# Kernel tuning notes

Measured on AMD Instinct MI355X. Metric: run time of the kernel, lower is better.

The kernel has to match this reference:

```python
import jax, jax.numpy as jnp
import numpy as np

BETA = 0.25


def setup_inputs() -> dict:
    key = jax.random.key(0)
    k1, k2 = jax.random.split(key)
    ze = jax.random.normal(k1, (16, 64, 64, 64), dtype=jnp.float32)  # (B, L, H, W)
    # codebook init mirrors uniform_(-1/K, 1/K)
    K = 1024
    emb = jax.random.uniform(k2, (K, 64), dtype=jnp.float32, minval=-1.0 / K, maxval=1.0 / K)
    return {"ze": ze, "emb": emb}


def reference(ze, emb):
    B, L, H, W = ze.shape
    K = emb.shape[0]
    # (B, H, W, L) -> (N, L)
    zf = jnp.transpose(ze, (0, 2, 3, 1)).reshape(-1, L)
    # squared euclidean distances (N, K)
    d = (jnp.sum(zf * zf, axis=1, keepdims=True)
         + jnp.sum(emb * emb, axis=1)
         - 2.0 * zf @ emb.T)
    idx = jnp.argmin(d, axis=1)  # (N,)
    # direct gather == one-hot @ emb
    z_q = jnp.transpose(emb[idx].reshape(B, H, W, L), (0, 3, 1, 2))
    loss = (jnp.mean((jax.lax.stop_gradient(z_q) - ze) ** 2)
            + BETA * jnp.mean((z_q - jax.lax.stop_gradient(ze)) ** 2))
    # straight-through estimator
    z_q_st = ze + jax.lax.stop_gradient(z_q - ze)
    # perplexity of code usage
    counts = jnp.zeros((K,), dtype=zf.dtype).at[idx].add(1.0)
    e_mean = counts / zf.shape[0]
    perplexity = jnp.exp(-jnp.sum(e_mean * jnp.log(e_mean + 1e-10)))
    return z_q_st, loss, idx.reshape(-1, 1)
```

## Files before the change

kernel.cpp:

```cpp
#include <hip/hip_runtime.h>

typedef short bf16x8 __attribute__((ext_vector_type(8)));
typedef float f32x4  __attribute__((ext_vector_type(4)));

#define CAP 12

#define WS_LOSS 0
#define WS_DONE 8
#define WS_EBF  64

#define L_EBF    0
#define L_MARG   131072
#define L_CCNT   132096
#define L_KCH    133120
#define L_ROWMAX 134144
#define L_CSLOT  136192
#define L_TOTAL  148480

__device__ __forceinline__ unsigned short f2bf(float f) {
    unsigned u = __float_as_uint(f);
    return (unsigned short)((u + 0x7fffu + ((u >> 16) & 1u)) >> 16);
}

__device__ __forceinline__ float np_pairwise_sumsq64(const float* a) {
    float r[8];
    #pragma unroll
    for (int j = 0; j < 8; ++j) r[j] = __fmul_rn(a[j], a[j]);
    #pragma unroll
    for (int i = 8; i < 64; i += 8)
        #pragma unroll
        for (int j = 0; j < 8; ++j)
            r[j] = __fadd_rn(r[j], __fmul_rn(a[i + j], a[i + j]));
    return __fadd_rn(
        __fadd_rn(__fadd_rn(r[0], r[1]), __fadd_rn(r[2], r[3])),
        __fadd_rn(__fadd_rn(r[4], r[5]), __fadd_rn(r[6], r[7])));
}

__global__ __launch_bounds__(256) void prep_kernel(
    const float* __restrict__ emb, unsigned short* __restrict__ ebf,
    float* __restrict__ loss, int* __restrict__ done)
{
    int k = blockIdx.x * 256 + threadIdx.x;
    if (k == 0) { *loss = 0.0f; *done = 0; }
    if (k < 1024) {
        float e[64];
        #pragma unroll
        for (int l = 0; l < 64; ++l) e[l] = emb[k * 64 + l];
        int tile = k >> 4, r = k & 15;
        #pragma unroll
        for (int j = 0; j < 8; ++j) {
            bf16x8 v;
            #pragma unroll
            for (int m = 0; m < 8; ++m) v[m] = (short)f2bf(e[j * 8 + m]);
            *(bf16x8*)(ebf + tile * 1024 + j * 128 + r * 8) = v;
        }
    }
}

__global__ __launch_bounds__(512)
__attribute__((amdgpu_waves_per_eu(2, 2)))
void vq_kernel(
    const float* __restrict__ ze, const float* __restrict__ emb,
    const unsigned short* __restrict__ ebf,
    float* __restrict__ out_zq, float* __restrict__ out_idxf,
    float* __restrict__ loss, int* __restrict__ done,
    float* __restrict__ out_loss)
{
    extern __shared__ char smem[];
    unsigned short* ebf_l   = (unsigned short*)(smem + L_EBF);
    float*          marg_l  = (float*)(smem + L_MARG);
    int*            ccnt    = (int*)(smem + L_CCNT);
    int*            kch     = (int*)(smem + L_KCH);
    float*          rowmax2 = (float*)(smem + L_ROWMAX);
    int*            cslot   = (int*)(smem + L_CSLOT);

    const int t = threadIdx.x;
    const int n0 = blockIdx.x * 256;
    const int gbase = (n0 >> 12) * 262144 + (n0 & 4095);

    if (t < 256) {
        const float* zp = ze + gbase + t;
        float S = 0.0f;
        #pragma unroll
        for (int l = 0; l < 64; ++l) S += fabsf(zp[l * 4096]);
        marg_l[t] = 1.67e-5f * S + 2.0e-4f;
        ccnt[t] = 0;
    } else {
        const int tt = t - 256;
        const bf16x8* src = (const bf16x8*)ebf;
        bf16x8* dst = (bf16x8*)ebf_l;
        #pragma unroll 8
        for (int i = 0; i < 32; ++i) dst[tt + i * 256] = src[tt + i * 256];
    }

    const int wv = t >> 6, lane = t & 63;
    const int r = lane & 15, q = lane >> 4;
    const int pg = wv & 3, kh = wv >> 2;
    const int wp = pg * 64;
    bf16x8 a0[4], a1[4];
    #pragma unroll
    for (int rg = 0; rg < 4; ++rg) {
        const float* zb = ze + gbase + wp + rg * 16 + r;
        #pragma unroll
        for (int j = 0; j < 8; ++j) {
            a0[rg][j] = (short)f2bf(zb[(q * 8 + j) * 4096]);
            a1[rg][j] = (short)f2bf(zb[(32 + q * 8 + j) * 4096]);
        }
    }
    __syncthreads();

    const unsigned short* bptr = ebf_l + (kh * 32) * 1024 + q * 128 + r * 8;

    float rm[16];
    #pragma unroll
    for (int i = 0; i < 16; ++i) rm[i] = -1e30f;
    {
        bf16x8 pb0[2], pb1[2];
        pb0[0] = *(const bf16x8*)(bptr);
        pb1[0] = *(const bf16x8*)(bptr + 512);
        pb0[1] = *(const bf16x8*)(bptr + 1024);
        pb1[1] = *(const bf16x8*)(bptr + 1536);
        #pragma unroll 4
        for (int tile = 0; tile < 32; ++tile) {
            bf16x8 b0 = pb0[tile & 1], b1 = pb1[tile & 1];
            int nt = tile + 2; if (nt > 31) nt = 31;
            pb0[tile & 1] = *(const bf16x8*)(bptr + nt * 1024);
            pb1[tile & 1] = *(const bf16x8*)(bptr + nt * 1024 + 512);
            #pragma unroll
            for (int rg = 0; rg < 4; ++rg) {
                f32x4 c = {0.f, 0.f, 0.f, 0.f};
                c = __builtin_amdgcn_mfma_f32_16x16x32_bf16(a0[rg], b0, c, 0, 0, 0);
                c = __builtin_amdgcn_mfma_f32_16x16x32_bf16(a1[rg], b1, c, 0, 0, 0);
                #pragma unroll
                for (int i = 0; i < 4; ++i)
                    rm[rg * 4 + i] = fmaxf(rm[rg * 4 + i], c[i]);
            }
        }
    }
    #pragma unroll
    for (int j = 0; j < 16; ++j) {
        float v = rm[j];
        v = fmaxf(v, __shfl_xor(v, 1, 16));
        v = fmaxf(v, __shfl_xor(v, 2, 16));
        v = fmaxf(v, __shfl_xor(v, 4, 16));
        v = fmaxf(v, __shfl_xor(v, 8, 16));
        int row = wp + (j >> 2) * 16 + q * 4 + (j & 3);
        if (r == 0) rowmax2[row * 2 + kh] = v;
    }
    __syncthreads();

    float thr[16];
    #pragma unroll
    for (int j = 0; j < 16; ++j) {
        int row = wp + (j >> 2) * 16 + q * 4 + (j & 3);
        thr[j] = fmaxf(rowmax2[row * 2], rowmax2[row * 2 + 1]) - 0.5f * marg_l[row];
    }

    {
        bf16x8 pb0[2], pb1[2];
        pb0[0] = *(const bf16x8*)(bptr);
        pb1[0] = *(const bf16x8*)(bptr + 512);
        pb0[1] = *(const bf16x8*)(bptr + 1024);
        pb1[1] = *(const bf16x8*)(bptr + 1536);
        #pragma unroll 4
        for (int tile = 0; tile < 32; ++tile) {
            bf16x8 b0 = pb0[tile & 1], b1 = pb1[tile & 1];
            int nt = tile + 2; if (nt > 31) nt = 31;
            pb0[tile & 1] = *(const bf16x8*)(bptr + nt * 1024);
            pb1[tile & 1] = *(const bf16x8*)(bptr + nt * 1024 + 512);
            int code = kh * 512 + tile * 16 + r;
            #pragma unroll
            for (int rg = 0; rg < 4; ++rg) {
                f32x4 c = {0.f, 0.f, 0.f, 0.f};
                c = __builtin_amdgcn_mfma_f32_16x16x32_bf16(a0[rg], b0, c, 0, 0, 0);
                c = __builtin_amdgcn_mfma_f32_16x16x32_bf16(a1[rg], b1, c, 0, 0, 0);
                #pragma unroll
                for (int i = 0; i < 4; ++i) {
                    if (c[i] >= thr[rg * 4 + i]) {
                        int pp = wp + rg * 16 + q * 4 + i;
                        int ci = atomicAdd(&ccnt[pp], 1);
                        if (ci < CAP) cslot[pp * CAP + ci] = code;
                    }
                }
            }
        }
    }
    __syncthreads();

    if (t < 256) {
        float z[64];
        const float* zp = ze + gbase + t;
        #pragma unroll
        for (int l = 0; l < 64; ++l) z[l] = zp[l * 4096];
        float znorm = np_pairwise_sumsq64(z);
        int cnt = ccnt[t]; if (cnt > CAP) cnt = CAP;
        float best = 1e30f; int bk = 1 << 20;
        for (int c = 0; c < cnt; ++c) {
            int k = cslot[t * CAP + c];
            float e[64];
            const float4* er = (const float4*)(emb + k * 64);
            #pragma unroll
            for (int j = 0; j < 16; ++j) {
                float4 v = er[j];
                e[4*j] = v.x; e[4*j+1] = v.y; e[4*j+2] = v.z; e[4*j+3] = v.w;
            }
            float en = np_pairwise_sumsq64(e);
            float acc = 0.0f;
            #pragma unroll
            for (int l = 0; l < 64; ++l) acc = fmaf(z[l], e[l], acc);
            float sc = __fsub_rn(__fadd_rn(znorm, en), __fmul_rn(2.0f, acc));
            if (sc < best || (sc == best && k < bk)) { best = sc; bk = k; }
        }
        kch[t] = bk;
        out_idxf[n0 + t] = (float)bk;
    }
    __syncthreads();

    {
        const int p = t & 255, h = t >> 8;
        const int bk = kch[p];
        const float* er = emb + bk * 64 + h * 32;
        const float* zp = ze + gbase + p + (h * 32) * 4096;
        float* op = out_zq + gbase + p + (h * 32) * 4096;
        float ls = 0.0f;
        #pragma unroll
        for (int j = 0; j < 32; ++j) {
            float qv = er[j];
            float zv = zp[j * 4096];
            op[j * 4096] = qv;
            float d = qv - zv;
            ls = fmaf(d, d, ls);
        }
        #pragma unroll
        for (int off = 32; off > 0; off >>= 1) ls += __shfl_down(ls, off, 64);
        if (lane == 0) atomicAdd(loss, ls);
    }

    __syncthreads();
    if (t == 0) {
        __threadfence();
        int old = atomicAdd(done, 1);
        if (old == (int)gridDim.x - 1) {
            __threadfence();
            float total = atomicAdd(loss, 0.0f);
            *out_loss = 1.25f * total / 4194304.0f;
        }
    }
}

extern "C" void kernel_launch(void* const* d_in, const int* in_sizes, int n_in,
                              void* d_out, int out_size, void* d_ws, size_t ws_size,
                              hipStream_t stream)
{
    const float* ze  = (const float*)d_in[0];
    const float* emb = (const float*)d_in[1];
    float* out = (float*)d_out;
    float* out_zq   = out;
    float* out_loss = out + 4194304;
    float* out_idxf = out + 4194305;

    char* w = (char*)d_ws;
    float*          ws_loss = (float*)(w + WS_LOSS);
    int*            ws_done = (int*)(w + WS_DONE);
    unsigned short* ebf     = (unsigned short*)(w + WS_EBF);

    static bool attr_set = false;
    if (!attr_set) {
        hipFuncSetAttribute((const void*)vq_kernel,
                            hipFuncAttributeMaxDynamicSharedMemorySize, L_TOTAL);
        attr_set = true;
    }

    prep_kernel<<<4, 256, 0, stream>>>(emb, ebf, ws_loss, ws_done);
    vq_kernel<<<256, 512, L_TOTAL, stream>>>(ze, emb, ebf, out_zq, out_idxf,
                                             ws_loss, ws_done, out_loss);
}
```

Before: 137.9 us.

## Shrink blocks to 64 points, stream bf16 codebook from global, stage ze in LDS

Restructures the VQ kernel from 256 blocks of 512 threads (256 points each, whole bf16 codebook copied into 128KB LDS) to 1024 blocks of 256 threads handling 64 points. Each wave now covers a quarter of the codebook and reads its B fragments directly from global/L2 with a deeper 4-stage register prefetch. The ze tile is staged once into padded LDS and reused for the margin, the MFMA operands, the rescoring and the loss, instead of being reloaded from global. Exact rescoring is split across 4 threads per point with an LDS reduction. The aim is more blocks and higher occupancy with a small LDS footprint, at the cost of repeated codebook reads through the cache.

```diff
diff --git a/kernel.cpp b/kernel.cpp
--- a/kernel.cpp
+++ b/kernel.cpp
@@ -9,13 +9,15 @@
 #define WS_DONE 8
 #define WS_EBF  64
 
-#define L_EBF    0
-#define L_MARG   131072
-#define L_CCNT   132096
-#define L_KCH    133120
-#define L_ROWMAX 134144
-#define L_CSLOT  136192
-#define L_TOTAL  148480
+#define L_ZL     0
+#define L_MARG   16640
+#define L_CCNT   16896
+#define L_KCH    17152
+#define L_RM4    17408
+#define L_CBS    18432
+#define L_CBK    19456
+#define L_CSLOT  20480
+#define L_TOTAL  23552
 
 __device__ __forceinline__ unsigned short f2bf(float f) {
     unsigned u = __float_as_uint(f);
@@ -57,8 +59,8 @@
     }
 }
 
-__global__ __launch_bounds__(512)
-__attribute__((amdgpu_waves_per_eu(2, 2)))
+__global__ __launch_bounds__(256)
+__attribute__((amdgpu_waves_per_eu(4)))
 void vq_kernel(
     const float* __restrict__ ze, const float* __restrict__ emb,
     const unsigned short* __restrict__ ebf,
@@ -67,65 +69,72 @@
     float* __restrict__ out_loss)
 {
     extern __shared__ char smem[];
-    unsigned short* ebf_l   = (unsigned short*)(smem + L_EBF);
-    float*          marg_l  = (float*)(smem + L_MARG);
-    int*            ccnt    = (int*)(smem + L_CCNT);
-    int*            kch     = (int*)(smem + L_KCH);
-    float*          rowmax2 = (float*)(smem + L_ROWMAX);
-    int*            cslot   = (int*)(smem + L_CSLOT);
+    float* zl     = (float*)(smem + L_ZL);
+    float* marg_l = (float*)(smem + L_MARG);
+    int*   ccnt   = (int*)(smem + L_CCNT);
+    int*   kch    = (int*)(smem + L_KCH);
+    float* rm4    = (float*)(smem + L_RM4);
+    float* cbs    = (float*)(smem + L_CBS);
+    int*   cbk    = (int*)(smem + L_CBK);
+    int*   cslot  = (int*)(smem + L_CSLOT);
 
     const int t = threadIdx.x;
-    const int n0 = blockIdx.x * 256;
+    const int n0 = blockIdx.x * 64;
     const int gbase = (n0 >> 12) * 262144 + (n0 & 4095);
 
-    if (t < 256) {
-        const float* zp = ze + gbase + t;
+    {
+        const int p4 = (t & 15) * 4, lg = t >> 4;
+        #pragma unroll
+        for (int i = 0; i < 4; ++i) {
+            const int l = lg + i * 16;
+            const float4 v = *(const float4*)(ze + gbase + l * 4096 + p4);
+            zl[l * 65 + p4 + 0] = v.x;
+            zl[l * 65 + p4 + 1] = v.y;
+            zl[l * 65 + p4 + 2] = v.z;
+            zl[l * 65 + p4 + 3] = v.w;
+        }
+        if (t < 64) ccnt[t] = 0;
+    }
+    __syncthreads();
+
+    if (t < 64) {
         float S = 0.0f;
         #pragma unroll
-        for (int l = 0; l < 64; ++l) S += fabsf(zp[l * 4096]);
+        for (int l = 0; l < 64; ++l) S += fabsf(zl[l * 65 + t]);
         marg_l[t] = 1.67e-5f * S + 2.0e-4f;
-        ccnt[t] = 0;
-    } else {
-        const int tt = t - 256;
-        const bf16x8* src = (const bf16x8*)ebf;
-        bf16x8* dst = (bf16x8*)ebf_l;
-        #pragma unroll 8
-        for (int i = 0; i < 32; ++i) dst[tt + i * 256] = src[tt + i * 256];
-    }
-
-    const int wv = t >> 6, lane = t & 63;
+    }
+
+    const int lane = t & 63, kq = t >> 6;
     const int r = lane & 15, q = lane >> 4;
-    const int pg = wv & 3, kh = wv >> 2;
-    const int wp = pg * 64;
+
     bf16x8 a0[4], a1[4];
     #pragma unroll
     for (int rg = 0; rg < 4; ++rg) {
-        const float* zb = ze + gbase + wp + rg * 16 + r;
         #pragma unroll
         for (int j = 0; j < 8; ++j) {
-            a0[rg][j] = (short)f2bf(zb[(q * 8 + j) * 4096]);
-            a1[rg][j] = (short)f2bf(zb[(32 + q * 8 + j) * 4096]);
-        }
-    }
-    __syncthreads();
-
-    const unsigned short* bptr = ebf_l + (kh * 32) * 1024 + q * 128 + r * 8;
+            a0[rg][j] = (short)f2bf(zl[(q * 8 + j) * 65 + rg * 16 + r]);
+            a1[rg][j] = (short)f2bf(zl[(32 + q * 8 + j) * 65 + rg * 16 + r]);
+        }
+    }
+
+    const unsigned short* gb = ebf + kq * 16384 + q * 128 + r * 8;
 
     float rm[16];
     #pragma unroll
     for (int i = 0; i < 16; ++i) rm[i] = -1e30f;
     {
-        bf16x8 pb0[2], pb1[2];
-        pb0[0] = *(const bf16x8*)(bptr);
-        pb1[0] = *(const bf16x8*)(bptr + 512);
-        pb0[1] = *(const bf16x8*)(bptr + 1024);
-        pb1[1] = *(const bf16x8*)(bptr + 1536);
+        bf16x8 pb0[4], pb1[4];
+        #pragma unroll
+        for (int i = 0; i < 4; ++i) {
+            pb0[i] = *(const bf16x8*)(gb + i * 1024);
+            pb1[i] = *(const bf16x8*)(gb + i * 1024 + 512);
+        }
         #pragma unroll 4
-        for (int tile = 0; tile < 32; ++tile) {
-            bf16x8 b0 = pb0[tile & 1], b1 = pb1[tile & 1];
-            int nt = tile + 2; if (nt > 31) nt = 31;
-            pb0[tile & 1] = *(const bf16x8*)(bptr + nt * 1024);
-            pb1[tile & 1] = *(const bf16x8*)(bptr + nt * 1024 + 512);
+        for (int tt = 0; tt < 16; ++tt) {
+            bf16x8 b0 = pb0[tt & 3], b1 = pb1[tt & 3];
+            int nt = tt + 4; if (nt > 15) nt = 15;
+            pb0[tt & 3] = *(const bf16x8*)(gb + nt * 1024);
+            pb1[tt & 3] = *(const bf16x8*)(gb + nt * 1024 + 512);
             #pragma unroll
             for (int rg = 0; rg < 4; ++rg) {
                 f32x4 c = {0.f, 0.f, 0.f, 0.f};
@@ -144,31 +153,34 @@
         v = fmaxf(v, __shfl_xor(v, 2, 16));
         v = fmaxf(v, __shfl_xor(v, 4, 16));
         v = fmaxf(v, __shfl_xor(v, 8, 16));
-        int row = wp + (j >> 2) * 16 + q * 4 + (j & 3);
-        if (r == 0) rowmax2[row * 2 + kh] = v;
+        const int row = (j >> 2) * 16 + q * 4 + (j & 3);
+        if (r == 0) rm4[row * 4 + kq] = v;
     }
     __syncthreads();
 
     float thr[16];
     #pragma unroll
     for (int j = 0; j < 16; ++j) {
-        int row = wp + (j >> 2) * 16 + q * 4 + (j & 3);
-        thr[j] = fmaxf(rowmax2[row * 2], rowmax2[row * 2 + 1]) - 0.5f * marg_l[row];
-    }
-
-    {
-        bf16x8 pb0[2], pb1[2];
-        pb0[0] = *(const bf16x8*)(bptr);
-        pb1[0] = *(const bf16x8*)(bptr + 512);
-        pb0[1] = *(const bf16x8*)(bptr + 1024);
-        pb1[1] = *(const bf16x8*)(bptr + 1536);
+        const int row = (j >> 2) * 16 + q * 4 + (j & 3);
+        const float maxc = fmaxf(fmaxf(rm4[row * 4 + 0], rm4[row * 4 + 1]),
+                                 fmaxf(rm4[row * 4 + 2], rm4[row * 4 + 3]));
+        thr[j] = maxc - 0.5f * marg_l[row];
+    }
+
+    {
+        bf16x8 pb0[4], pb1[4];
+        #pragma unroll
+        for (int i = 0; i < 4; ++i) {
+            pb0[i] = *(const bf16x8*)(gb + i * 1024);
+            pb1[i] = *(const bf16x8*)(gb + i * 1024 + 512);
+        }
         #pragma unroll 4
-        for (int tile = 0; tile < 32; ++tile) {
-            bf16x8 b0 = pb0[tile & 1], b1 = pb1[tile & 1];
-            int nt = tile + 2; if (nt > 31) nt = 31;
-            pb0[tile & 1] = *(const bf16x8*)(bptr + nt * 1024);
-            pb1[tile & 1] = *(const bf16x8*)(bptr + nt * 1024 + 512);
-            int code = kh * 512 + tile * 16 + r;
+        for (int tt = 0; tt < 16; ++tt) {
+            bf16x8 b0 = pb0[tt & 3], b1 = pb1[tt & 3];
+            int nt = tt + 4; if (nt > 15) nt = 15;
+            pb0[tt & 3] = *(const bf16x8*)(gb + nt * 1024);
+            pb1[tt & 3] = *(const bf16x8*)(gb + nt * 1024 + 512);
+            const int code = kq * 256 + tt * 16 + r;
             #pragma unroll
             for (int rg = 0; rg < 4; ++rg) {
                 f32x4 c = {0.f, 0.f, 0.f, 0.f};
@@ -177,8 +189,8 @@
                 #pragma unroll
                 for (int i = 0; i < 4; ++i) {
                     if (c[i] >= thr[rg * 4 + i]) {
-                        int pp = wp + rg * 16 + q * 4 + i;
-                        int ci = atomicAdd(&ccnt[pp], 1);
+                        const int pp = rg * 16 + q * 4 + i;
+                        const int ci = atomicAdd(&ccnt[pp], 1);
                         if (ci < CAP) cslot[pp * CAP + ci] = code;
                     }
                 }
@@ -187,16 +199,16 @@
     }
     __syncthreads();
 
-    if (t < 256) {
+    {
+        const int p = t & 63, cl = t >> 6;
+        int cnt = ccnt[p]; if (cnt > CAP) cnt = CAP;
         float z[64];
-        const float* zp = ze + gbase + t;
-        #pragma unroll
-        for (int l = 0; l < 64; ++l) z[l] = zp[l * 4096];
-        float znorm = np_pairwise_sumsq64(z);
-        int cnt = ccnt[t]; if (cnt > CAP) cnt = CAP;
+        #pragma unroll
+        for (int l = 0; l < 64; ++l) z[l] = zl[l * 65 + p];
+        const float znorm = np_pairwise_sumsq64(z);
         float best = 1e30f; int bk = 1 << 20;
-        for (int c = 0; c < cnt; ++c) {
-            int k = cslot[t * CAP + c];
+        for (int c = cl; c < cnt; c += 4) {
+            const int k = cslot[p * CAP + c];
             float e[64];
             const float4* er = (const float4*)(emb + k * 64);
             #pragma unroll
@@ -204,11 +216,23 @@
                 float4 v = er[j];
                 e[4*j] = v.x; e[4*j+1] = v.y; e[4*j+2] = v.z; e[4*j+3] = v.w;
             }
-            float en = np_pairwise_sumsq64(e);
+            const float en = np_pairwise_sumsq64(e);
             float acc = 0.0f;
             #pragma unroll
             for (int l = 0; l < 64; ++l) acc = fmaf(z[l], e[l], acc);
-            float sc = __fsub_rn(__fadd_rn(znorm, en), __fmul_rn(2.0f, acc));
+            const float sc = __fsub_rn(__fadd_rn(znorm, en), __fmul_rn(2.0f, acc));
+            if (sc < best || (sc == best && k < bk)) { best = sc; bk = k; }
+        }
+        cbs[cl * 64 + p] = best;
+        cbk[cl * 64 + p] = bk;
+    }
+    __syncthreads();
+
+    if (t < 64) {
+        float best = cbs[t]; int bk = cbk[t];
+        #pragma unroll
+        for (int i = 1; i < 4; ++i) {
+            const float sc = cbs[i * 64 + t]; const int k = cbk[i * 64 + t];
             if (sc < best || (sc == best && k < bk)) { best = sc; bk = k; }
         }
         kch[t] = bk;
@@ -217,18 +241,17 @@
     __syncthreads();
 
     {
-        const int p = t & 255, h = t >> 8;
+        const int p = t & 63, h = t >> 6;
         const int bk = kch[p];
-        const float* er = emb + bk * 64 + h * 32;
-        const float* zp = ze + gbase + p + (h * 32) * 4096;
-        float* op = out_zq + gbase + p + (h * 32) * 4096;
+        const float* er = emb + bk * 64 + h * 16;
+        float* op = out_zq + gbase + p + (h * 16) * 4096;
         float ls = 0.0f;
         #pragma unroll
-        for (int j = 0; j < 32; ++j) {
-            float qv = er[j];
-            float zv = zp[j * 4096];
+        for (int j = 0; j < 16; ++j) {
+            const float qv = er[j];
+            const float zv = zl[(h * 16 + j) * 65 + p];
             op[j * 4096] = qv;
-            float d = qv - zv;
+            const float d = qv - zv;
             ls = fmaf(d, d, ls);
         }
         #pragma unroll
@@ -264,14 +287,7 @@
     int*            ws_done = (int*)(w + WS_DONE);
     unsigned short* ebf     = (unsigned short*)(w + WS_EBF);
 
-    static bool attr_set = false;
-    if (!attr_set) {
-        hipFuncSetAttribute((const void*)vq_kernel,
-                            hipFuncAttributeMaxDynamicSharedMemorySize, L_TOTAL);
-        attr_set = true;
-    }
-
     prep_kernel<<<4, 256, 0, stream>>>(emb, ebf, ws_loss, ws_done);
-    vq_kernel<<<256, 512, L_TOTAL, stream>>>(ze, emb, ebf, out_zq, out_idxf,
-                                             ws_loss, ws_done, out_loss);
-}
+    vq_kernel<<<1024, 256, L_TOTAL, stream>>>(ze, emb, ebf, out_zq, out_idxf,
+                                              ws_loss, ws_done, out_loss);
+}
```

Result: slower. 162.2 us (+17.6%).

## Double block size to 1024 threads, split codebook four ways and parallelize rescoring

Applied to the files above, without the earlier changes.

Raises the block size from 512 to 1024 threads, so each wave scans a quarter of the codebook instead of half, and row maxima are merged across four partial results. The exact fp32 candidate rescoring, which used only 256 threads, is now spread across all 1024 threads (four candidate lanes per point) with a shared-memory argmin reduction afterwards. The output write and loss pass also uses all threads. This aims to raise parallelism and shorten the serial rescoring tail. In exchange each thread gets fewer registers (launch bounds 1024), which may cause spills given the large A-fragment and z arrays, and an extra barrier is added.

```diff
diff --git a/kernel.cpp b/kernel.cpp
--- a/kernel.cpp
+++ b/kernel.cpp
@@ -13,27 +13,15 @@
 #define L_MARG   131072
 #define L_CCNT   132096
 #define L_KCH    133120
-#define L_ROWMAX 134144
-#define L_CSLOT  136192
-#define L_TOTAL  148480
+#define L_RM4    134144
+#define L_CSLOT  138240
+#define L_CBS    150528
+#define L_CBK    154624
+#define L_TOTAL  158720
 
 __device__ __forceinline__ unsigned short f2bf(float f) {
     unsigned u = __float_as_uint(f);
     return (unsigned short)((u + 0x7fffu + ((u >> 16) & 1u)) >> 16);
-}
-
-__device__ __forceinline__ float np_pairwise_sumsq64(const float* a) {
-    float r[8];
-    #pragma unroll
-    for (int j = 0; j < 8; ++j) r[j] = __fmul_rn(a[j], a[j]);
-    #pragma unroll
-    for (int i = 8; i < 64; i += 8)
-        #pragma unroll
-        for (int j = 0; j < 8; ++j)
-            r[j] = __fadd_rn(r[j], __fmul_rn(a[i + j], a[i + j]));
-    return __fadd_rn(
-        __fadd_rn(__fadd_rn(r[0], r[1]), __fadd_rn(r[2], r[3])),
-        __fadd_rn(__fadd_rn(r[4], r[5]), __fadd_rn(r[6], r[7])));
 }
 
 __global__ __launch_bounds__(256) void prep_kernel(
@@ -57,8 +45,7 @@
     }
 }
 
-__global__ __launch_bounds__(512)
-__attribute__((amdgpu_waves_per_eu(2, 2)))
+__global__ __launch_bounds__(1024, 4)
 void vq_kernel(
     const float* __restrict__ ze, const float* __restrict__ emb,
     const unsigned short* __restrict__ ebf,
@@ -67,17 +54,25 @@
     float* __restrict__ out_loss)
 {
     extern __shared__ char smem[];
-    unsigned short* ebf_l   = (unsigned short*)(smem + L_EBF);
-    float*          marg_l  = (float*)(smem + L_MARG);
-    int*            ccnt    = (int*)(smem + L_CCNT);
-    int*            kch     = (int*)(smem + L_KCH);
-    float*          rowmax2 = (float*)(smem + L_ROWMAX);
-    int*            cslot   = (int*)(smem + L_CSLOT);
+    unsigned short* ebf_l = (unsigned short*)(smem + L_EBF);
+    float*          marg_l= (float*)(smem + L_MARG);
+    int*            ccnt  = (int*)(smem + L_CCNT);
+    int*            kch   = (int*)(smem + L_KCH);
+    float*          rm4   = (float*)(smem + L_RM4);
+    int*            cslot = (int*)(smem + L_CSLOT);
+    float*          cbs   = (float*)(smem + L_CBS);
+    int*            cbk   = (int*)(smem + L_CBK);
 
     const int t = threadIdx.x;
     const int n0 = blockIdx.x * 256;
     const int gbase = (n0 >> 12) * 262144 + (n0 & 4095);
 
+    {
+        const bf16x8* src = (const bf16x8*)ebf;
+        bf16x8* dst = (bf16x8*)ebf_l;
+        #pragma unroll 8
+        for (int i = 0; i < 8; ++i) dst[t + i * 1024] = src[t + i * 1024];
+    }
     if (t < 256) {
         const float* zp = ze + gbase + t;
         float S = 0.0f;
@@ -85,17 +80,11 @@
         for (int l = 0; l < 64; ++l) S += fabsf(zp[l * 4096]);
         marg_l[t] = 1.67e-5f * S + 2.0e-4f;
         ccnt[t] = 0;
-    } else {
-        const int tt = t - 256;
-        const bf16x8* src = (const bf16x8*)ebf;
-        bf16x8* dst = (bf16x8*)ebf_l;
-        #pragma unroll 8
-        for (int i = 0; i < 32; ++i) dst[tt + i * 256] = src[tt + i * 256];
     }
 
     const int wv = t >> 6, lane = t & 63;
     const int r = lane & 15, q = lane >> 4;
-    const int pg = wv & 3, kh = wv >> 2;
+    const int pg = wv & 3, kq = wv >> 2;
     const int wp = pg * 64;
     bf16x8 a0[4], a1[4];
     #pragma unroll
@@ -109,7 +98,7 @@
     }
     __syncthreads();
 
-    const unsigned short* bptr = ebf_l + (kh * 32) * 1024 + q * 128 + r * 8;
+    const unsigned short* bptr = ebf_l + (kq * 16) * 1024 + q * 128 + r * 8;
 
     float rm[16];
     #pragma unroll
@@ -121,9 +110,9 @@
         pb0[1] = *(const bf16x8*)(bptr + 1024);
         pb1[1] = *(const bf16x8*)(bptr + 1536);
         #pragma unroll 4
-        for (int tile = 0; tile < 32; ++tile) {
+        for (int tile = 0; tile < 16; ++tile) {
             bf16x8 b0 = pb0[tile & 1], b1 = pb1[tile & 1];
-            int nt = tile + 2; if (nt > 31) nt = 31;
+            int nt = tile + 2; if (nt > 15) nt = 15;
             pb0[tile & 1] = *(const bf16x8*)(bptr + nt * 1024);
             pb1[tile & 1] = *(const bf16x8*)(bptr + nt * 1024 + 512);
             #pragma unroll
@@ -144,16 +133,18 @@
         v = fmaxf(v, __shfl_xor(v, 2, 16));
         v = fmaxf(v, __shfl_xor(v, 4, 16));
         v = fmaxf(v, __shfl_xor(v, 8, 16));
-        int row = wp + (j >> 2) * 16 + q * 4 + (j & 3);
-        if (r == 0) rowmax2[row * 2 + kh] = v;
+        const int row = wp + (j >> 2) * 16 + q * 4 + (j & 3);
+        if (r == 0) rm4[row * 4 + kq] = v;
     }
     __syncthreads();
 
     float thr[16];
     #pragma unroll
     for (int j = 0; j < 16; ++j) {
-        int row = wp + (j >> 2) * 16 + q * 4 + (j & 3);
-        thr[j] = fmaxf(rowmax2[row * 2], rowmax2[row * 2 + 1]) - 0.5f * marg_l[row];
+        const int row = wp + (j >> 2) * 16 + q * 4 + (j & 3);
+        const float maxc = fmaxf(fmaxf(rm4[row * 4 + 0], rm4[row * 4 + 1]),
+                                 fmaxf(rm4[row * 4 + 2], rm4[row * 4 + 3]));
+        thr[j] = maxc - 0.5f * marg_l[row];
     }
 
     {
@@ -163,12 +154,12 @@
         pb0[1] = *(const bf16x8*)(bptr + 1024);
         pb1[1] = *(const bf16x8*)(bptr + 1536);
         #pragma unroll 4
-        for (int tile = 0; tile < 32; ++tile) {
+        for (int tile = 0; tile < 16; ++tile) {
             bf16x8 b0 = pb0[tile & 1], b1 = pb1[tile & 1];
-            int nt = tile + 2; if (nt > 31) nt = 31;
+            int nt = tile + 2; if (nt > 15) nt = 15;
             pb0[tile & 1] = *(const bf16x8*)(bptr + nt * 1024);
             pb1[tile & 1] = *(const bf16x8*)(bptr + nt * 1024 + 512);
-            int code = kh * 512 + tile * 16 + r;
+            const int code = kq * 256 + tile * 16 + r;
             #pragma unroll
             for (int rg = 0; rg < 4; ++rg) {
                 f32x4 c = {0.f, 0.f, 0.f, 0.f};
@@ -177,8 +168,8 @@
                 #pragma unroll
                 for (int i = 0; i < 4; ++i) {
                     if (c[i] >= thr[rg * 4 + i]) {
-                        int pp = wp + rg * 16 + q * 4 + i;
-                        int ci = atomicAdd(&ccnt[pp], 1);
+                        const int pp = wp + rg * 16 + q * 4 + i;
+                        const int ci = atomicAdd(&ccnt[pp], 1);
                         if (ci < CAP) cslot[pp * CAP + ci] = code;
                     }
                 }
@@ -187,28 +178,79 @@
     }
     __syncthreads();
 
+    {
+        const int p = t & 255, cl = t >> 8;
+        int cnt = ccnt[p]; if (cnt > CAP) cnt = CAP;
+        float z[64];
+        const float* zp = ze + gbase + p;
+        #pragma unroll
+        for (int l = 0; l < 64; ++l) z[l] = zp[l * 4096];
+        float znorm;
+        {
+            float rz[8];
+            #pragma unroll
+            for (int j = 0; j < 8; ++j) rz[j] = __fmul_rn(z[j], z[j]);
+            #pragma unroll
+            for (int i = 8; i < 64; i += 8)
+                #pragma unroll
+                for (int j = 0; j < 8; ++j)
+                    rz[j] = __fadd_rn(rz[j], __fmul_rn(z[i + j], z[i + j]));
+            znorm = __fadd_rn(
+                __fadd_rn(__fadd_rn(rz[0], rz[1]), __fadd_rn(rz[2], rz[3])),
+                __fadd_rn(__fadd_rn(rz[4], rz[5]), __fadd_rn(rz[6], rz[7])));
+        }
+        float best = 1e30f; int bk = 1 << 20;
+        for (int c = cl; c < cnt; c += 4) {
+            const int k = cslot[p * CAP + c];
+            const float4* er = (const float4*)(emb + k * 64);
+            float rr[8];
+            float acc = 0.0f;
+            #pragma unroll
+            for (int ch = 0; ch < 8; ++ch) {
+                const float4 va = er[2 * ch];
+                const float4 vb = er[2 * ch + 1];
+                float e0 = va.x, e1 = va.y, e2 = va.z, e3 = va.w;
+                float e4 = vb.x, e5 = vb.y, e6 = vb.z, e7 = vb.w;
+                if (ch == 0) {
+                    rr[0] = __fmul_rn(e0, e0); rr[1] = __fmul_rn(e1, e1);
+                    rr[2] = __fmul_rn(e2, e2); rr[3] = __fmul_rn(e3, e3);
+                    rr[4] = __fmul_rn(e4, e4); rr[5] = __fmul_rn(e5, e5);
+                    rr[6] = __fmul_rn(e6, e6); rr[7] = __fmul_rn(e7, e7);
+                } else {
+                    rr[0] = __fadd_rn(rr[0], __fmul_rn(e0, e0));
+                    rr[1] = __fadd_rn(rr[1], __fmul_rn(e1, e1));
+                    rr[2] = __fadd_rn(rr[2], __fmul_rn(e2, e2));
+                    rr[3] = __fadd_rn(rr[3], __fmul_rn(e3, e3));
+                    rr[4] = __fadd_rn(rr[4], __fmul_rn(e4, e4));
+                    rr[5] = __fadd_rn(rr[5], __fmul_rn(e5, e5));
+                    rr[6] = __fadd_rn(rr[6], __fmul_rn(e6, e6));
+                    rr[7] = __fadd_rn(rr[7], __fmul_rn(e7, e7));
+                }
+                acc = fmaf(z[8 * ch + 0], e0, acc);
+                acc = fmaf(z[8 * ch + 1], e1, acc);
+                acc = fmaf(z[8 * ch + 2], e2, acc);
+                acc = fmaf(z[8 * ch + 3], e3, acc);
+                acc = fmaf(z[8 * ch + 4], e4, acc);
+                acc = fmaf(z[8 * ch + 5], e5, acc);
+                acc = fmaf(z[8 * ch + 6], e6, acc);
+                acc = fmaf(z[8 * ch + 7], e7, acc);
+            }
+            const float en = __fadd_rn(
+                __fadd_rn(__fadd_rn(rr[0], rr[1]), __fadd_rn(rr[2], rr[3])),
+                __fadd_rn(__fadd_rn(rr[4], rr[5]), __fadd_rn(rr[6], rr[7])));
+            const float sc = __fsub_rn(__fadd_rn(znorm, en), __fmul_rn(2.0f, acc));
+            if (sc < best || (sc == best && k < bk)) { best = sc; bk = k; }
+        }
+        cbs[cl * 256 + p] = best;
+        cbk[cl * 256 + p] = bk;
+    }
+    __syncthreads();
+
     if (t < 256) {
-        float z[64];
-        const float* zp = ze + gbase + t;
-        #pragma unroll
-        for (int l = 0; l < 64; ++l) z[l] = zp[l * 4096];
-        float znorm = np_pairwise_sumsq64(z);
-        int cnt = ccnt[t]; if (cnt > CAP) cnt = CAP;
-        float best = 1e30f; int bk = 1 << 20;
-        for (int c = 0; c < cnt; ++c) {
-            int k = cslot[t * CAP + c];
-            float e[64];
-            const float4* er = (const float4*)(emb + k * 64);
-            #pragma unroll
-            for (int j = 0; j < 16; ++j) {
-                float4 v = er[j];
-                e[4*j] = v.x; e[4*j+1] = v.y; e[4*j+2] = v.z; e[4*j+3] = v.w;
-            }
-            float en = np_pairwise_sumsq64(e);
-            float acc = 0.0f;
-            #pragma unroll
-            for (int l = 0; l < 64; ++l) acc = fmaf(z[l], e[l], acc);
-            float sc = __fsub_rn(__fadd_rn(znorm, en), __fmul_rn(2.0f, acc));
+        float best = cbs[t]; int bk = cbk[t];
+        #pragma unroll
+        for (int i = 1; i < 4; ++i) {
+            const float sc = cbs[i * 256 + t]; const int k = cbk[i * 256 + t];
             if (sc < best || (sc == best && k < bk)) { best = sc; bk = k; }
         }
         kch[t] = bk;
@@ -219,16 +261,16 @@
     {
         const int p = t & 255, h = t >> 8;
         const int bk = kch[p];
-        const float* er = emb + bk * 64 + h * 32;
-        const float* zp = ze + gbase + p + (h * 32) * 4096;
-        float* op = out_zq + gbase + p + (h * 32) * 4096;
+        const float* er = emb + bk * 64 + h * 16;
+        const float* zp = ze + gbase + p + (h * 16) * 4096;
+        float* op = out_zq + gbase + p + (h * 16) * 4096;
         float ls = 0.0f;
         #pragma unroll
-        for (int j = 0; j < 32; ++j) {
-            float qv = er[j];
-            float zv = zp[j * 4096];
+        for (int j = 0; j < 16; ++j) {
+            const float qv = er[j];
+            const float zv = zp[j * 4096];
             op[j * 4096] = qv;
-            float d = qv - zv;
+            const float d = qv - zv;
             ls = fmaf(d, d, ls);
         }
         #pragma unroll
@@ -272,6 +314,6 @@
     }
 
     prep_kernel<<<4, 256, 0, stream>>>(emb, ebf, ws_loss, ws_done);
-    vq_kernel<<<256, 512, L_TOTAL, stream>>>(ze, emb, ebf, out_zq, out_idxf,
-                                             ws_loss, ws_done, out_loss);
+    vq_kernel<<<256, 1024, L_TOTAL, stream>>>(ze, emb, ebf, out_zq, out_idxf,
+                                              ws_loss, ws_done, out_loss);
 }
```

Result: slower. 160.1 us (+16.1%).

## Repartition waves over rows, precompute code norms, split rescoring across thread pairs

Applied to the files above, without the earlier changes.

Each of the 8 waves now owns 32 rows and sweeps all 1024 codes, where before 4 row-groups of 64 were split across two code halves. This removes the shared-memory rowmax exchange and the barrier between the max pass and the candidate pass. Codebook squared norms are now computed once in the prep kernel and read from workspace instead of being recomputed per candidate. Candidate rescoring uses all 512 threads, two per row with a shuffle-based merge, and the margin sums are computed from the same ze loads used for the MFMA operands. The cost is more LDS B-fragment reads per MFMA, since each wave covers fewer rows, and a deeper prefetch ring.

```diff
diff --git a/kernel.cpp b/kernel.cpp
--- a/kernel.cpp
+++ b/kernel.cpp
@@ -7,15 +7,15 @@
 
 #define WS_LOSS 0
 #define WS_DONE 8
-#define WS_EBF  64
+#define WS_EN   64
+#define WS_EBF  4160
 
 #define L_EBF    0
 #define L_MARG   131072
 #define L_CCNT   132096
 #define L_KCH    133120
-#define L_ROWMAX 134144
-#define L_CSLOT  136192
-#define L_TOTAL  148480
+#define L_CSLOT  134144
+#define L_TOTAL  146432
 
 __device__ __forceinline__ unsigned short f2bf(float f) {
     unsigned u = __float_as_uint(f);
@@ -38,6 +38,7 @@
 
 __global__ __launch_bounds__(256) void prep_kernel(
     const float* __restrict__ emb, unsigned short* __restrict__ ebf,
+    float* __restrict__ en_t,
     float* __restrict__ loss, int* __restrict__ done)
 {
     int k = blockIdx.x * 256 + threadIdx.x;
@@ -46,6 +47,7 @@
         float e[64];
         #pragma unroll
         for (int l = 0; l < 64; ++l) e[l] = emb[k * 64 + l];
+        en_t[k] = np_pairwise_sumsq64(e);
         int tile = k >> 4, r = k & 15;
         #pragma unroll
         for (int j = 0; j < 8; ++j) {
@@ -57,80 +59,82 @@
     }
 }
 
-__global__ __launch_bounds__(512)
-__attribute__((amdgpu_waves_per_eu(2, 2)))
+__global__ __launch_bounds__(512, 2)
 void vq_kernel(
     const float* __restrict__ ze, const float* __restrict__ emb,
-    const unsigned short* __restrict__ ebf,
+    const unsigned short* __restrict__ ebf, const float* __restrict__ en_t,
     float* __restrict__ out_zq, float* __restrict__ out_idxf,
     float* __restrict__ loss, int* __restrict__ done,
     float* __restrict__ out_loss)
 {
     extern __shared__ char smem[];
-    unsigned short* ebf_l   = (unsigned short*)(smem + L_EBF);
-    float*          marg_l  = (float*)(smem + L_MARG);
-    int*            ccnt    = (int*)(smem + L_CCNT);
-    int*            kch     = (int*)(smem + L_KCH);
-    float*          rowmax2 = (float*)(smem + L_ROWMAX);
-    int*            cslot   = (int*)(smem + L_CSLOT);
+    unsigned short* ebf_l = (unsigned short*)(smem + L_EBF);
+    float*          marg_l= (float*)(smem + L_MARG);
+    int*            ccnt  = (int*)(smem + L_CCNT);
+    int*            kch   = (int*)(smem + L_KCH);
+    int*            cslot = (int*)(smem + L_CSLOT);
 
     const int t = threadIdx.x;
     const int n0 = blockIdx.x * 256;
     const int gbase = (n0 >> 12) * 262144 + (n0 & 4095);
 
-    if (t < 256) {
-        const float* zp = ze + gbase + t;
-        float S = 0.0f;
-        #pragma unroll
-        for (int l = 0; l < 64; ++l) S += fabsf(zp[l * 4096]);
-        marg_l[t] = 1.67e-5f * S + 2.0e-4f;
-        ccnt[t] = 0;
-    } else {
-        const int tt = t - 256;
+    {
         const bf16x8* src = (const bf16x8*)ebf;
         bf16x8* dst = (bf16x8*)ebf_l;
-        #pragma unroll 8
-        for (int i = 0; i < 32; ++i) dst[tt + i * 256] = src[tt + i * 256];
+        #pragma unroll 16
+        for (int i = 0; i < 16; ++i) dst[t + i * 512] = src[t + i * 512];
     }
 
     const int wv = t >> 6, lane = t & 63;
     const int r = lane & 15, q = lane >> 4;
-    const int pg = wv & 3, kh = wv >> 2;
-    const int wp = pg * 64;
-    bf16x8 a0[4], a1[4];
-    #pragma unroll
-    for (int rg = 0; rg < 4; ++rg) {
+    const int wp = wv * 32;
+    bf16x8 a[2][2];
+    float sm[2] = {0.f, 0.f};
+    #pragma unroll
+    for (int rg = 0; rg < 2; ++rg) {
         const float* zb = ze + gbase + wp + rg * 16 + r;
         #pragma unroll
         for (int j = 0; j < 8; ++j) {
-            a0[rg][j] = (short)f2bf(zb[(q * 8 + j) * 4096]);
-            a1[rg][j] = (short)f2bf(zb[(32 + q * 8 + j) * 4096]);
-        }
-    }
-    __syncthreads();
-
-    const unsigned short* bptr = ebf_l + (kh * 32) * 1024 + q * 128 + r * 8;
-
-    float rm[16];
-    #pragma unroll
-    for (int i = 0; i < 16; ++i) rm[i] = -1e30f;
-    {
-        bf16x8 pb0[2], pb1[2];
-        pb0[0] = *(const bf16x8*)(bptr);
-        pb1[0] = *(const bf16x8*)(bptr + 512);
-        pb0[1] = *(const bf16x8*)(bptr + 1024);
-        pb1[1] = *(const bf16x8*)(bptr + 1536);
+            const float v0 = zb[(q * 8 + j) * 4096];
+            const float v1 = zb[(32 + q * 8 + j) * 4096];
+            a[rg][0][j] = (short)f2bf(v0);
+            a[rg][1][j] = (short)f2bf(v1);
+            sm[rg] += fabsf(v0) + fabsf(v1);
+        }
+    }
+    #pragma unroll
+    for (int rg = 0; rg < 2; ++rg) {
+        float s = sm[rg];
+        s += __shfl_xor(s, 16, 64);
+        s += __shfl_xor(s, 32, 64);
+        if (q == 0) marg_l[wp + rg * 16 + r] = 1.67e-5f * s + 2.0e-4f;
+    }
+    if (t < 256) ccnt[t] = 0;
+    __syncthreads();
+
+    const unsigned short* bptr = ebf_l + q * 128 + r * 8;
+
+    float rm[8];
+    #pragma unroll
+    for (int i = 0; i < 8; ++i) rm[i] = -1e30f;
+    {
+        bf16x8 pb0[4], pb1[4];
+        #pragma unroll
+        for (int i = 0; i < 4; ++i) {
+            pb0[i] = *(const bf16x8*)(bptr + i * 1024);
+            pb1[i] = *(const bf16x8*)(bptr + i * 1024 + 512);
+        }
         #pragma unroll 4
-        for (int tile = 0; tile < 32; ++tile) {
-            bf16x8 b0 = pb0[tile & 1], b1 = pb1[tile & 1];
-            int nt = tile + 2; if (nt > 31) nt = 31;
-            pb0[tile & 1] = *(const bf16x8*)(bptr + nt * 1024);
-            pb1[tile & 1] = *(const bf16x8*)(bptr + nt * 1024 + 512);
-            #pragma unroll
-            for (int rg = 0; rg < 4; ++rg) {
+        for (int tile = 0; tile < 64; ++tile) {
+            bf16x8 b0 = pb0[tile & 3], b1 = pb1[tile & 3];
+            int nt = tile + 4; if (nt > 63) nt = 63;
+            pb0[tile & 3] = *(const bf16x8*)(bptr + nt * 1024);
+            pb1[tile & 3] = *(const bf16x8*)(bptr + nt * 1024 + 512);
+            #pragma unroll
+            for (int rg = 0; rg < 2; ++rg) {
                 f32x4 c = {0.f, 0.f, 0.f, 0.f};
-                c = __builtin_amdgcn_mfma_f32_16x16x32_bf16(a0[rg], b0, c, 0, 0, 0);
-                c = __builtin_amdgcn_mfma_f32_16x16x32_bf16(a1[rg], b1, c, 0, 0, 0);
+                c = __builtin_amdgcn_mfma_f32_16x16x32_bf16(a[rg][0], b0, c, 0, 0, 0);
+                c = __builtin_amdgcn_mfma_f32_16x16x32_bf16(a[rg][1], b1, c, 0, 0, 0);
                 #pragma unroll
                 for (int i = 0; i < 4; ++i)
                     rm[rg * 4 + i] = fmaxf(rm[rg * 4 + i], c[i]);
@@ -138,47 +142,45 @@
         }
     }
     #pragma unroll
-    for (int j = 0; j < 16; ++j) {
+    for (int j = 0; j < 8; ++j) {
         float v = rm[j];
         v = fmaxf(v, __shfl_xor(v, 1, 16));
         v = fmaxf(v, __shfl_xor(v, 2, 16));
         v = fmaxf(v, __shfl_xor(v, 4, 16));
         v = fmaxf(v, __shfl_xor(v, 8, 16));
-        int row = wp + (j >> 2) * 16 + q * 4 + (j & 3);
-        if (r == 0) rowmax2[row * 2 + kh] = v;
-    }
-    __syncthreads();
-
-    float thr[16];
-    #pragma unroll
-    for (int j = 0; j < 16; ++j) {
-        int row = wp + (j >> 2) * 16 + q * 4 + (j & 3);
-        thr[j] = fmaxf(rowmax2[row * 2], rowmax2[row * 2 + 1]) - 0.5f * marg_l[row];
-    }
-
-    {
-        bf16x8 pb0[2], pb1[2];
-        pb0[0] = *(const bf16x8*)(bptr);
-        pb1[0] = *(const bf16x8*)(bptr + 512);
-        pb0[1] = *(const bf16x8*)(bptr + 1024);
-        pb1[1] = *(const bf16x8*)(bptr + 1536);
+        rm[j] = v;
+    }
+    float thr[8];
+    #pragma unroll
+    for (int j = 0; j < 8; ++j) {
+        const int row = wp + (j >> 2) * 16 + q * 4 + (j & 3);
+        thr[j] = rm[j] - 0.5f * marg_l[row];
+    }
+
+    {
+        bf16x8 pb0[4], pb1[4];
+        #pragma unroll
+        for (int i = 0; i < 4; ++i) {
+            pb0[i] = *(const bf16x8*)(bptr + i * 1024);
+            pb1[i] = *(const bf16x8*)(bptr + i * 1024 + 512);
+        }
         #pragma unroll 4
-        for (int tile = 0; tile < 32; ++tile) {
-            bf16x8 b0 = pb0[tile & 1], b1 = pb1[tile & 1];
-            int nt = tile + 2; if (nt > 31) nt = 31;
-            pb0[tile & 1] = *(const bf16x8*)(bptr + nt * 1024);
-            pb1[tile & 1] = *(const bf16x8*)(bptr + nt * 1024 + 512);
-            int code = kh * 512 + tile * 16 + r;
-            #pragma unroll
-            for (int rg = 0; rg < 4; ++rg) {
+        for (int tile = 0; tile < 64; ++tile) {
+            bf16x8 b0 = pb0[tile & 3], b1 = pb1[tile & 3];
+            int nt = tile + 4; if (nt > 63) nt = 63;
+            pb0[tile & 3] = *(const bf16x8*)(bptr + nt * 1024);
+            pb1[tile & 3] = *(const bf16x8*)(bptr + nt * 1024 + 512);
+            const int code = tile * 16 + r;
+            #pragma unroll
+            for (int rg = 0; rg < 2; ++rg) {
                 f32x4 c = {0.f, 0.f, 0.f, 0.f};
-                c = __builtin_amdgcn_mfma_f32_16x16x32_bf16(a0[rg], b0, c, 0, 0, 0);
-                c = __builtin_amdgcn_mfma_f32_16x16x32_bf16(a1[rg], b1, c, 0, 0, 0);
+                c = __builtin_amdgcn_mfma_f32_16x16x32_bf16(a[rg][0], b0, c, 0, 0, 0);
+                c = __builtin_amdgcn_mfma_f32_16x16x32_bf16(a[rg][1], b1, c, 0, 0, 0);
                 #pragma unroll
                 for (int i = 0; i < 4; ++i) {
                     if (c[i] >= thr[rg * 4 + i]) {
-                        int pp = wp + rg * 16 + q * 4 + i;
-                        int ci = atomicAdd(&ccnt[pp], 1);
+                        const int pp = wp + rg * 16 + q * 4 + i;
+                        const int ci = atomicAdd(&ccnt[pp], 1);
                         if (ci < CAP) cslot[pp * CAP + ci] = code;
                     }
                 }
@@ -187,32 +189,37 @@
     }
     __syncthreads();
 
-    if (t < 256) {
+    {
+        const int p = t >> 1, cl = t & 1;
+        int cnt = ccnt[p]; if (cnt > CAP) cnt = CAP;
         float z[64];
-        const float* zp = ze + gbase + t;
+        const float* zp = ze + gbase + p;
         #pragma unroll
         for (int l = 0; l < 64; ++l) z[l] = zp[l * 4096];
-        float znorm = np_pairwise_sumsq64(z);
-        int cnt = ccnt[t]; if (cnt > CAP) cnt = CAP;
+        const float znorm = np_pairwise_sumsq64(z);
         float best = 1e30f; int bk = 1 << 20;
-        for (int c = 0; c < cnt; ++c) {
-            int k = cslot[t * CAP + c];
-            float e[64];
+        for (int c = cl; c < cnt; c += 2) {
+            const int k = cslot[p * CAP + c];
             const float4* er = (const float4*)(emb + k * 64);
-            #pragma unroll
-            for (int j = 0; j < 16; ++j) {
-                float4 v = er[j];
-                e[4*j] = v.x; e[4*j+1] = v.y; e[4*j+2] = v.z; e[4*j+3] = v.w;
+            float acc = 0.0f;
+            #pragma unroll
+            for (int jj = 0; jj < 16; ++jj) {
+                const float4 v = er[jj];
+                acc = fmaf(z[4 * jj + 0], v.x, acc);
+                acc = fmaf(z[4 * jj + 1], v.y, acc);
+                acc = fmaf(z[4 * jj + 2], v.z, acc);
+                acc = fmaf(z[4 * jj + 3], v.w, acc);
             }
-            float en = np_pairwise_sumsq64(e);
-            float acc = 0.0f;
-            #pragma unroll
-            for (int l = 0; l < 64; ++l) acc = fmaf(z[l], e[l], acc);
-            float sc = __fsub_rn(__fadd_rn(znorm, en), __fmul_rn(2.0f, acc));
+            const float sc = __fsub_rn(__fadd_rn(znorm, en_t[k]), __fmul_rn(2.0f, acc));
             if (sc < best || (sc == best && k < bk)) { best = sc; bk = k; }
         }
-        kch[t] = bk;
-        out_idxf[n0 + t] = (float)bk;
+        const float ob = __shfl_xor(best, 1, 64);
+        const int   ok = __shfl_xor(bk, 1, 64);
+        if (ob < best || (ob == best && ok < bk)) { best = ob; bk = ok; }
+        if (cl == 0) {
+            kch[p] = bk;
+            out_idxf[n0 + p] = (float)bk;
+        }
     }
     __syncthreads();
 
@@ -225,10 +232,10 @@
         float ls = 0.0f;
         #pragma unroll
         for (int j = 0; j < 32; ++j) {
-            float qv = er[j];
-            float zv = zp[j * 4096];
+            const float qv = er[j];
+            const float zv = zp[j * 4096];
             op[j * 4096] = qv;
-            float d = qv - zv;
+            const float d = qv - zv;
             ls = fmaf(d, d, ls);
         }
         #pragma unroll
@@ -262,6 +269,7 @@
     char* w = (char*)d_ws;
     float*          ws_loss = (float*)(w + WS_LOSS);
     int*            ws_done = (int*)(w + WS_DONE);
+    float*          ws_en   = (float*)(w + WS_EN);
     unsigned short* ebf     = (unsigned short*)(w + WS_EBF);
 
     static bool attr_set = false;
@@ -271,7 +279,7 @@
         attr_set = true;
     }
 
-    prep_kernel<<<4, 256, 0, stream>>>(emb, ebf, ws_loss, ws_done);
-    vq_kernel<<<256, 512, L_TOTAL, stream>>>(ze, emb, ebf, out_zq, out_idxf,
-                                             ws_loss, ws_done, out_loss);
-}
+    prep_kernel<<<4, 256, 0, stream>>>(emb, ebf, ws_en, ws_loss, ws_done);
+    vq_kernel<<<256, 512, L_TOTAL, stream>>>(ze, emb, ebf, ws_en, out_zq,
+                                             out_idxf, ws_loss, ws_done, out_loss);
+}
```

Measured after the change: 140.0 us. No clear change (+1.5%).
